# Kernel optimization log

Hardware: AMD Instinct MI355X
Metric: run time of the kernel (lower is better)

Reference implementation:

```python
import jax, jax.numpy as jnp
import numpy as np

BETA = 0.001       # gamma of the soft-min
THRESHOLD = 2.0    # padding cost for 'skip' slots


def _build_cost(centers_a, centers_b):
    # sort by timestamp (last column), then drop it (keep_times=False)
    a = centers_a[jnp.argsort(centers_a[:, -1])][:, :-1]
    b = centers_b[jnp.argsort(centers_b[:, -1])][:, :-1]
    a = a / jnp.sqrt(jnp.sum(a * a, axis=-1, keepdims=True) + 1e-10)
    b = b / jnp.sqrt(jnp.sum(b * b, axis=-1, keepdims=True) + 1e-10)
    cost = 1.0 - a @ b.T                      # [M, N] cosine cost
    M, N = cost.shape
    # interleave real costs with threshold 'skip' columns: [M, 2N]
    c2 = jnp.concatenate([cost, jnp.full_like(cost, THRESHOLD)], axis=0)  # [2M, N]
    c3 = c2.T.reshape(2 * N, M).T                                         # [M, 2N]
    c4 = jnp.concatenate(
        [jnp.full((M, 1), THRESHOLD, dtype=cost.dtype), c3], axis=1)      # [M, 2N+1]
    return jax.nn.softmax(c4, axis=-1)  # softmax='row'


def _dwsa_loss(C, gamma):
    # C: [M, K] with K = 2N+1. DP: D[i,j] = softmin(D[i-1, :p_j]) + C[i,j]
    # where p_j = j+1 for even j, j for odd j (prefix soft-min of previous row).
    M, K = C.shape
    j = jnp.arange(K)
    idx = jnp.where(j % 2 == 0, j, j - 1)  # inclusive prefix end index

    def step(d_prev, c_row):
        # stable prefix soft-min via cumulative logsumexp of -D/gamma
        lcse = jax.lax.cumlogsumexp(-d_prev / gamma)   # [K]
        softmin = -gamma * lcse[idx]                   # [K]
        d = softmin + c_row
        return d, None

    d_last, _ = jax.lax.scan(step, C[0], C[1:])
    # final soft-min over last row
    return -gamma * jax.nn.logsumexp(-d_last / gamma)


def setup_inputs() -> dict:
    key = jax.random.key(0)
    k1, k2 = jax.random.split(key)
    centers_a = jax.random.normal(k1, (2048, 513), dtype=jnp.float32)
    centers_b = jax.random.normal(k2, (2048, 513), dtype=jnp.float32)
    return {"centers_a": centers_a, "centers_b": centers_b}


def reference(centers_a, centers_b):
    C = _build_cost(centers_a, centers_b)
    return _dwsa_loss(C, BETA)
```

## Files before the change

### kernel.cpp

```cpp
#include <hip/hip_runtime.h>
#include <math.h>

#define M_ROWS 2048
#define N_COLS 2048
#define DIMS 512
#define IN_STRIDE 513
#define DP_BLOCKS 32
#define DP_COLS 64
#define BAND 16

constexpr float GAMMA = 0.001f;
constexpr float LOG2E = 1.44269504088896f;
constexpr float LN2   = 0.69314718055995f;

__device__ __forceinline__ float fexp2(float x) { return __builtin_amdgcn_exp2f(x); }
__device__ __forceinline__ float flog2(float x) { return __builtin_amdgcn_logf(x); }

__device__ __forceinline__ unsigned short f2bf(float x) {
    unsigned u = __float_as_uint(x);
    return (unsigned short)((u + 0x7FFFu + ((u >> 16) & 1u)) >> 16);
}
__device__ __forceinline__ float bf2f(unsigned short u) {
    return __uint_as_float((unsigned)u << 16);
}

__global__ void argsort_kernel(const float* __restrict__ a, const float* __restrict__ b,
                               int* __restrict__ permA, int* __restrict__ permB) {
    const float* src = blockIdx.y ? b : a;
    int* perm = blockIdx.y ? permB : permA;
    __shared__ float keys[M_ROWS];
    for (int j = threadIdx.x; j < M_ROWS; j += blockDim.x)
        keys[j] = src[(size_t)j * IN_STRIDE + DIMS];
    __syncthreads();
    int i = blockIdx.x * blockDim.x + threadIdx.x;
    float ki = keys[i];
    int rank = 0;
    for (int j = 0; j < M_ROWS; ++j) {
        float kj = keys[j];
        rank += (kj < ki) || (kj == ki && j < i);
    }
    perm[rank] = i;
}

__global__ __launch_bounds__(128) void norm_kernel(const float* __restrict__ a, const float* __restrict__ b,
                                                   const int* __restrict__ permA, const int* __restrict__ permB,
                                                   unsigned short* __restrict__ Ahi, unsigned short* __restrict__ Alo,
                                                   unsigned short* __restrict__ Bhi, unsigned short* __restrict__ Blo) {
    const float* src = blockIdx.y ? b : a;
    const int* perm = blockIdx.y ? permB : permA;
    unsigned short* dhi = blockIdx.y ? Bhi : Ahi;
    unsigned short* dlo = blockIdx.y ? Blo : Alo;
    int r = blockIdx.x;
    int row = perm[r];
    const float* p = src + (size_t)row * IN_STRIDE;
    int tid = threadIdx.x;
    float v0 = p[tid], v1 = p[tid + 128], v2 = p[tid + 256], v3 = p[tid + 384];
    float ss = v0 * v0 + v1 * v1 + v2 * v2 + v3 * v3;
    #pragma unroll
    for (int off = 32; off > 0; off >>= 1) ss += __shfl_down(ss, off);
    __shared__ float red[2];
    if ((tid & 63) == 0) red[tid >> 6] = ss;
    __syncthreads();
    float inv = 1.0f / sqrtf(red[0] + red[1] + 1e-10f);
    unsigned short* qh = dhi + (size_t)r * DIMS;
    unsigned short* ql = dlo + (size_t)r * DIMS;
    float x;
    unsigned short h;
    x = v0 * inv; h = f2bf(x); qh[tid]       = h; ql[tid]       = f2bf(x - bf2f(h));
    x = v1 * inv; h = f2bf(x); qh[tid + 128] = h; ql[tid + 128] = f2bf(x - bf2f(h));
    x = v2 * inv; h = f2bf(x); qh[tid + 256] = h; ql[tid + 256] = f2bf(x - bf2f(h));
    x = v3 * inv; h = f2bf(x); qh[tid + 384] = h; ql[tid + 384] = f2bf(x - bf2f(h));
}

typedef __attribute__((ext_vector_type(8))) short bf16x8;
typedef __attribute__((ext_vector_type(4))) float f32x4;

__global__ __launch_bounds__(256) void gemm_kernel(const unsigned short* __restrict__ Ahi,
                                                   const unsigned short* __restrict__ Alo,
                                                   const unsigned short* __restrict__ Bhi,
                                                   const unsigned short* __restrict__ Blo,
                                                   float* __restrict__ Q) {
    const int tid = threadIdx.x;
    const int lane = tid & 63;
    const int wv = tid >> 6;
    const int row0 = blockIdx.y * 64 + (wv >> 1) * 32;
    const int col0 = blockIdx.x * 64 + (wv & 1) * 32;
    const int lr = lane & 15;
    const int kj = (lane >> 4) * 8;
    const size_t ar0 = (size_t)(row0 + lr) * DIMS + kj;
    const size_t ar1 = (size_t)(row0 + 16 + lr) * DIMS + kj;
    const size_t br0 = (size_t)(col0 + lr) * DIMS + kj;
    const size_t br1 = (size_t)(col0 + 16 + lr) * DIMS + kj;
    f32x4 acc00 = {}, acc01 = {}, acc10 = {}, acc11 = {};
    for (int k0 = 0; k0 < DIMS; k0 += 32) {
        bf16x8 a0h = *(const bf16x8*)(Ahi + ar0 + k0);
        bf16x8 a1h = *(const bf16x8*)(Ahi + ar1 + k0);
        bf16x8 a0l = *(const bf16x8*)(Alo + ar0 + k0);
        bf16x8 a1l = *(const bf16x8*)(Alo + ar1 + k0);
        bf16x8 b0h = *(const bf16x8*)(Bhi + br0 + k0);
        bf16x8 b1h = *(const bf16x8*)(Bhi + br1 + k0);
        bf16x8 b0l = *(const bf16x8*)(Blo + br0 + k0);
        bf16x8 b1l = *(const bf16x8*)(Blo + br1 + k0);
        acc00 = __builtin_amdgcn_mfma_f32_16x16x32_bf16(a0l, b0h, acc00, 0, 0, 0);
        acc00 = __builtin_amdgcn_mfma_f32_16x16x32_bf16(a0h, b0l, acc00, 0, 0, 0);
        acc00 = __builtin_amdgcn_mfma_f32_16x16x32_bf16(a0h, b0h, acc00, 0, 0, 0);
        acc01 = __builtin_amdgcn_mfma_f32_16x16x32_bf16(a0l, b1h, acc01, 0, 0, 0);
        acc01 = __builtin_amdgcn_mfma_f32_16x16x32_bf16(a0h, b1l, acc01, 0, 0, 0);
        acc01 = __builtin_amdgcn_mfma_f32_16x16x32_bf16(a0h, b1h, acc01, 0, 0, 0);
        acc10 = __builtin_amdgcn_mfma_f32_16x16x32_bf16(a1l, b0h, acc10, 0, 0, 0);
        acc10 = __builtin_amdgcn_mfma_f32_16x16x32_bf16(a1h, b0l, acc10, 0, 0, 0);
        acc10 = __builtin_amdgcn_mfma_f32_16x16x32_bf16(a1h, b0h, acc10, 0, 0, 0);
        acc11 = __builtin_amdgcn_mfma_f32_16x16x32_bf16(a1l, b1h, acc11, 0, 0, 0);
        acc11 = __builtin_amdgcn_mfma_f32_16x16x32_bf16(a1h, b1l, acc11, 0, 0, 0);
        acc11 = __builtin_amdgcn_mfma_f32_16x16x32_bf16(a1h, b1h, acc11, 0, 0, 0);
    }
    const int rbase = (lane >> 4) * 4;
    #pragma unroll
    for (int r = 0; r < 4; ++r) {
        Q[(size_t)(row0 + rbase + r) * N_COLS + col0 + lr]           = __expf(-1.0f - acc00[r]);
        Q[(size_t)(row0 + rbase + r) * N_COLS + col0 + 16 + lr]      = __expf(-1.0f - acc01[r]);
        Q[(size_t)(row0 + 16 + rbase + r) * N_COLS + col0 + lr]      = __expf(-1.0f - acc10[r]);
        Q[(size_t)(row0 + 16 + rbase + r) * N_COLS + col0 + 16 + lr] = __expf(-1.0f - acc11[r]);
    }
}

__global__ __launch_bounds__(256) void rowstat_kernel(const float* __restrict__ Q,
                                                      float* __restrict__ rowscale,
                                                      float* __restrict__ ews) {
    int i = blockIdx.x;
    const float* q = Q + (size_t)i * N_COLS;
    int tid = threadIdx.x;
    float4 x = *(const float4*)(q + tid * 4);
    float4 y = *(const float4*)(q + 1024 + tid * 4);
    float s = x.x + x.y + x.z + x.w + y.x + y.y + y.z + y.w;
    #pragma unroll
    for (int off = 32; off > 0; off >>= 1) s += __shfl_down(s, off);
    __shared__ float red[4];
    if ((tid & 63) == 0) red[tid >> 6] = s;
    __syncthreads();
    if (tid == 0) {
        float denom = 2049.0f + red[0] + red[1] + red[2] + red[3];
        float rs = (LOG2E / GAMMA) / denom;
        rowscale[i] = rs;
        ews[i] = fexp2(-rs);
    }
}

__global__ __launch_bounds__(256) void lgt_kernel(const float* __restrict__ Q,
                                                  const float* __restrict__ rowscale,
                                                  float* __restrict__ ELT) {
    __shared__ float tile[64][65];
    const int row0 = blockIdx.y * 64;
    const int col0 = blockIdx.x * 64;
    const int t = threadIdx.x;
    const int c4 = (t & 15) * 4;
    const int r  = t >> 4;
    #pragma unroll
    for (int rr = 0; rr < 64; rr += 16) {
        int row = row0 + rr + r;
        float rs = rowscale[row];
        float4 v = *(const float4*)(Q + (size_t)row * N_COLS + col0 + c4);
        float e = fexp2(-rs);
        tile[c4 + 0][rr + r] = e + fexp2(-rs * v.x);
        tile[c4 + 1][rr + r] = e + fexp2(-rs * v.y);
        tile[c4 + 2][rr + r] = e + fexp2(-rs * v.z);
        tile[c4 + 3][rr + r] = e + fexp2(-rs * v.w);
    }
    __syncthreads();
    #pragma unroll
    for (int cc = 0; cc < 64; cc += 16) {
        int col = cc + r;
        float4 o;
        o.x = tile[col][c4 + 0];
        o.y = tile[col][c4 + 1];
        o.z = tile[col][c4 + 2];
        o.w = tile[col][c4 + 3];
        *(float4*)(ELT + (size_t)(col0 + col) * M_ROWS + row0 + c4) = o;
    }
}

#define KEEP4(v) asm volatile("" : "+v"(v.x), "+v"(v.y), "+v"(v.z), "+v"(v.w))

#define SST(V, MODS) asm("s_nop 1\n\tv_add_f32_dpp %0, %0, %0 " MODS : "+v"(V))
#define SCAN6                                                            \
    SST(t, "row_shr:1 row_mask:0xf bank_mask:0xf bound_ctrl:0");         \
    SST(t, "row_shr:2 row_mask:0xf bank_mask:0xf bound_ctrl:0");         \
    SST(t, "row_shr:4 row_mask:0xf bank_mask:0xf bound_ctrl:0");         \
    SST(t, "row_shr:8 row_mask:0xf bank_mask:0xf bound_ctrl:0");         \
    SST(t, "row_bcast:15 row_mask:0xa bank_mask:0xf bound_ctrl:0");      \
    SST(t, "row_bcast:31 row_mask:0xc bank_mask:0xf bound_ctrl:0")

#define DP_ROW(U, ELV, EWV, VCI)                                                 \
    {                                                                            \
        float ci = 0.f;                                                          \
        if (s > 0)                                                               \
            ci = __int_as_float(__builtin_amdgcn_readlane(                       \
                     __float_as_int(VCI), (U)));                                 \
        float t = w * (ELV);                                                     \
        float pre = fmaf(w, (EWV) - (ELV), ci);                                  \
        SCAN6;                                                                   \
        float all = ci + t;                                                      \
        float wn = pre + t;                                                      \
        if (s < DP_BLOCKS - 1) {                                                 \
            if (lane == 63) {                                                    \
                unsigned long long po =                                          \
                    ((unsigned long long)__float_as_uint(all) << 32)             \
                    | (unsigned long long)__float_as_uint(Rm);                   \
                __hip_atomic_store(pub + base + (U), po, __ATOMIC_RELAXED,       \
                                   __HIP_MEMORY_SCOPE_AGENT);                    \
            }                                                                    \
        } else {                                                                 \
            h = fmaf(h, (EWV), all);                                             \
        }                                                                        \
        w = wn;                                                                  \
    }

#define RENORM8                                                                  \
    {                                                                            \
        int e48 = __builtin_amdgcn_readlane(__builtin_amdgcn_frexp_expf(w), 48); \
        float f = __int_as_float((127 - e48) << 23);                             \
        w *= f; h *= f;                                                          \
        Rm += (float)e48;                                                        \
    }

#define WAIT_BAND                                                                \
    if (s > 0) {                                                                 \
        for (;;) {                                                               \
            unsigned long long miss = __ballot((lane < BAND) && pk == 0ull);     \
            if (miss == 0ull) break;                                             \
            if (pk == 0ull && lane < BAND)                                       \
                pk = __hip_atomic_load(sub + base + lane, __ATOMIC_RELAXED,      \
                                       __HIP_MEMORY_SCOPE_AGENT);               \
        }                                                                        \
        pkLo = (int)(unsigned)(pk & 0xFFFFFFFFull);                              \
        pkHi = (int)(unsigned)(pk >> 32);                                        \
    }

__global__ __launch_bounds__(64) void dp_kernel(const float* __restrict__ ELT,
                                                const float* __restrict__ Ews,
                                                unsigned long long* __restrict__ carry,
                                                float* __restrict__ out) {
    const int s = ((blockIdx.x & 7) << 2) | (blockIdx.x >> 3);
    const int lane = threadIdx.x;
    const float* lcol = ELT + (size_t)(s * DP_COLS + lane) * M_ROWS;
    unsigned long long* pub = carry + (size_t)s * M_ROWS;
    const unsigned long long* sub = carry + (size_t)(s - 1) * M_ROWS;

    float w = 1.f;
    float Rm = 0.f;
    float h = 1.f;

    float4 lq0 = *(const float4*)(lcol + 0);
    float4 lq1 = *(const float4*)(lcol + 4);
    float4 lq2 = *(const float4*)(lcol + 8);
    float4 lq3 = *(const float4*)(lcol + 12);
    float4 ev0 = *(const float4*)(Ews + 0);
    float4 ev1 = *(const float4*)(Ews + 4);
    float4 ev2 = *(const float4*)(Ews + 8);
    float4 ev3 = *(const float4*)(Ews + 12);
    KEEP4(lq0); KEEP4(lq1); KEEP4(lq2); KEEP4(lq3);
    KEEP4(ev0); KEEP4(ev1); KEEP4(ev2); KEEP4(ev3);

    unsigned long long pk = 1ull;
    if (s > 0 && lane < BAND)
        pk = __hip_atomic_load(sub + lane, __ATOMIC_RELAXED, __HIP_MEMORY_SCOPE_AGENT);

    for (int base = 0; base < M_ROWS; base += BAND) {
        float4 nl0{}, nl1{}, nl2{}, nl3{}, nv0{}, nv1{}, nv2{}, nv3{};
        if (base + BAND < M_ROWS) {
            nl0 = *(const float4*)(lcol + base + BAND);
            nl1 = *(const float4*)(lcol + base + BAND + 4);
            nl2 = *(const float4*)(lcol + base + BAND + 8);
            nl3 = *(const float4*)(lcol + base + BAND + 12);
            nv0 = *(const float4*)(Ews + base + BAND);
            nv1 = *(const float4*)(Ews + base + BAND + 4);
            nv2 = *(const float4*)(Ews + base + BAND + 8);
            nv3 = *(const float4*)(Ews + base + BAND + 12);
        }
        KEEP4(nl0); KEEP4(nl1); KEEP4(nl2); KEEP4(nl3);
        KEEP4(nv0); KEEP4(nv1); KEEP4(nv2); KEEP4(nv3);

        int pkLo = 0, pkHi = 0;
        WAIT_BAND
        float vci01 = 0.f;
        if (s > 0)
            vci01 = __int_as_float(pkHi) * fexp2(
                __int_as_float(__builtin_amdgcn_readlane(pkLo, 0)) - Rm);

        DP_ROW(0,  lq0.x, ev0.x, vci01)
        DP_ROW(1,  lq0.y, ev0.y, vci01)
        DP_ROW(2,  lq0.z, ev0.z, vci01)
        DP_ROW(3,  lq0.w, ev0.w, vci01)
        DP_ROW(4,  lq1.x, ev1.x, vci01)
        DP_ROW(5,  lq1.y, ev1.y, vci01)
        DP_ROW(6,  lq1.z, ev1.z, vci01)
        DP_ROW(7,  lq1.w, ev1.w, vci01)
        RENORM8
        float vci23 = 0.f;
        if (s > 0)
            vci23 = __int_as_float(pkHi) * fexp2(
                __int_as_float(__builtin_amdgcn_readlane(pkLo, 8)) - Rm);
        unsigned long long nk = 1ull;
        if (s > 0 && lane < BAND && base + BAND < M_ROWS)
            nk = __hip_atomic_load(sub + base + BAND + lane,
                                   __ATOMIC_RELAXED, __HIP_MEMORY_SCOPE_AGENT);

        DP_ROW(8,  lq2.x, ev2.x, vci23)
        DP_ROW(9,  lq2.y, ev2.y, vci23)
        DP_ROW(10, lq2.z, ev2.z, vci23)
        DP_ROW(11, lq2.w, ev2.w, vci23)
        DP_ROW(12, lq3.x, ev3.x, vci23)
        DP_ROW(13, lq3.y, ev3.y, vci23)
        DP_ROW(14, lq3.z, ev3.z, vci23)
        DP_ROW(15, lq3.w, ev3.w, vci23)
        RENORM8
        pk = nk;

        lq0 = nl0; lq1 = nl1; lq2 = nl2; lq3 = nl3;
        ev0 = nv0; ev1 = nv1; ev2 = nv2; ev3 = nv3;
    }
    if (s == DP_BLOCKS - 1 && lane == 63)
        out[0] = -GAMMA * LN2 * (Rm + flog2(h));
}

extern "C" void kernel_launch(void* const* d_in, const int* in_sizes, int n_in,
                              void* d_out, int out_size, void* d_ws, size_t ws_size,
                              hipStream_t stream) {
    (void)in_sizes; (void)n_in; (void)out_size; (void)ws_size;
    const float* a = (const float*)d_in[0];
    const float* b = (const float*)d_in[1];
    float* out = (float*)d_out;
    char* ws = (char*)d_ws;
    float* Q        = (float*)(ws);
    float* ELT      = (float*)(ws + (size_t)16 * 1024 * 1024);
    unsigned short* Ahi = (unsigned short*)(ws + (size_t)32 * 1024 * 1024);
    unsigned short* Alo = (unsigned short*)(ws + (size_t)34 * 1024 * 1024);
    unsigned short* Bhi = (unsigned short*)(ws + (size_t)36 * 1024 * 1024);
    unsigned short* Blo = (unsigned short*)(ws + (size_t)38 * 1024 * 1024);
    float* rowscale = (float*)(ws + (size_t)40 * 1024 * 1024);
    int* permA      = (int*)(ws + (size_t)40 * 1024 * 1024 + 8192);
    int* permB      = (int*)(ws + (size_t)40 * 1024 * 1024 + 16384);
    float* ews      = (float*)(ws + (size_t)40 * 1024 * 1024 + 24576);
    unsigned long long* carry = (unsigned long long*)(ws + (size_t)41 * 1024 * 1024);

    hipMemsetAsync(carry, 0, (size_t)DP_BLOCKS * M_ROWS * sizeof(unsigned long long), stream);
    argsort_kernel<<<dim3(8, 2), 256, 0, stream>>>(a, b, permA, permB);
    norm_kernel<<<dim3(2048, 2), 128, 0, stream>>>(a, b, permA, permB, Ahi, Alo, Bhi, Blo);
    gemm_kernel<<<dim3(32, 32), 256, 0, stream>>>(Ahi, Alo, Bhi, Blo, Q);
    rowstat_kernel<<<2048, 256, 0, stream>>>(Q, rowscale, ews);
    lgt_kernel<<<dim3(32, 32), 256, 0, stream>>>(Q, rowscale, ELT);
    dp_kernel<<<DP_BLOCKS, DP_COLS, 0, stream>>>(ELT, ews, carry, out);
}
```

Before: 582.4 us.

## Split DP band wait into halves, vectorize norm I/O, defer prefetch fences

The wavefront DP now waits only for the first eight carry values from the previous column block before starting, and polls for the second half during the first eight rows. This lets each block begin earlier in the pipeline. The norm kernel reads four contiguous floats per thread and writes ushort4 vectors, and the readlane of the carry is no longer guarded on s>0. The KEEP4 register fences are moved after the band so the prefetch loads can complete later. The changed carry handshake risks subtle ordering issues, and the unguarded readlane relies on vci being zero for block 0.

```diff
diff --git a/kernel.cpp b/kernel.cpp
--- a/kernel.cpp
+++ b/kernel.cpp
@@ -54,7 +54,7 @@
     int row = perm[r];
     const float* p = src + (size_t)row * IN_STRIDE;
     int tid = threadIdx.x;
-    float v0 = p[tid], v1 = p[tid + 128], v2 = p[tid + 256], v3 = p[tid + 384];
+    float v0 = p[4 * tid], v1 = p[4 * tid + 1], v2 = p[4 * tid + 2], v3 = p[4 * tid + 3];
     float ss = v0 * v0 + v1 * v1 + v2 * v2 + v3 * v3;
     #pragma unroll
     for (int off = 32; off > 0; off >>= 1) ss += __shfl_down(ss, off);
@@ -62,14 +62,14 @@
     if ((tid & 63) == 0) red[tid >> 6] = ss;
     __syncthreads();
     float inv = 1.0f / sqrtf(red[0] + red[1] + 1e-10f);
-    unsigned short* qh = dhi + (size_t)r * DIMS;
-    unsigned short* ql = dlo + (size_t)r * DIMS;
-    float x;
-    unsigned short h;
-    x = v0 * inv; h = f2bf(x); qh[tid]       = h; ql[tid]       = f2bf(x - bf2f(h));
-    x = v1 * inv; h = f2bf(x); qh[tid + 128] = h; ql[tid + 128] = f2bf(x - bf2f(h));
-    x = v2 * inv; h = f2bf(x); qh[tid + 256] = h; ql[tid + 256] = f2bf(x - bf2f(h));
-    x = v3 * inv; h = f2bf(x); qh[tid + 384] = h; ql[tid + 384] = f2bf(x - bf2f(h));
+    float x0 = v0 * inv, x1 = v1 * inv, x2 = v2 * inv, x3 = v3 * inv;
+    ushort4 hv, lv;
+    hv.x = f2bf(x0); lv.x = f2bf(x0 - bf2f(hv.x));
+    hv.y = f2bf(x1); lv.y = f2bf(x1 - bf2f(hv.y));
+    hv.z = f2bf(x2); lv.z = f2bf(x2 - bf2f(hv.z));
+    hv.w = f2bf(x3); lv.w = f2bf(x3 - bf2f(hv.w));
+    *(ushort4*)(dhi + (size_t)r * DIMS + 4 * tid) = hv;
+    *(ushort4*)(dlo + (size_t)r * DIMS + 4 * tid) = lv;
 }
 
 typedef __attribute__((ext_vector_type(8))) short bf16x8;
@@ -192,10 +192,8 @@
 
 #define DP_ROW(U, ELV, EWV, VCI)                                                 \
     {                                                                            \
-        float ci = 0.f;                                                          \
-        if (s > 0)                                                               \
-            ci = __int_as_float(__builtin_amdgcn_readlane(                       \
-                     __float_as_int(VCI), (U)));                                 \
+        float ci = __int_as_float(__builtin_amdgcn_readlane(                     \
+                       __float_as_int(VCI), (U)));                               \
         float t = w * (ELV);                                                     \
         float pre = fmaf(w, (EWV) - (ELV), ci);                                  \
         SCAN6;                                                                   \
@@ -223,12 +221,13 @@
         Rm += (float)e48;                                                        \
     }
 
-#define WAIT_BAND                                                                \
+#define WAIT_HALF(hh)                                                            \
     if (s > 0) {                                                                 \
         for (;;) {                                                               \
-            unsigned long long miss = __ballot((lane < BAND) && pk == 0ull);     \
+            unsigned long long miss =                                            \
+                __ballot(((lane >> 3) == (hh)) && pk == 0ull);                   \
             if (miss == 0ull) break;                                             \
-            if (pk == 0ull && lane < BAND)                                       \
+            if (pk == 0ull && lane < BAND && (lane >> 3) >= (hh))                \
                 pk = __hip_atomic_load(sub + base + lane, __ATOMIC_RELAXED,      \
                                        __HIP_MEMORY_SCOPE_AGENT);               \
         }                                                                        \
@@ -277,11 +276,9 @@
             nv2 = *(const float4*)(Ews + base + BAND + 8);
             nv3 = *(const float4*)(Ews + base + BAND + 12);
         }
-        KEEP4(nl0); KEEP4(nl1); KEEP4(nl2); KEEP4(nl3);
-        KEEP4(nv0); KEEP4(nv1); KEEP4(nv2); KEEP4(nv3);
 
         int pkLo = 0, pkHi = 0;
-        WAIT_BAND
+        WAIT_HALF(0)
         float vci01 = 0.f;
         if (s > 0)
             vci01 = __int_as_float(pkHi) * fexp2(
@@ -290,24 +287,28 @@
         DP_ROW(0,  lq0.x, ev0.x, vci01)
         DP_ROW(1,  lq0.y, ev0.y, vci01)
         DP_ROW(2,  lq0.z, ev0.z, vci01)
+        if (s > 0 && pk == 0ull && (lane >> 3) == 1)
+            pk = __hip_atomic_load(sub + base + lane, __ATOMIC_RELAXED,
+                                   __HIP_MEMORY_SCOPE_AGENT);
         DP_ROW(3,  lq0.w, ev0.w, vci01)
         DP_ROW(4,  lq1.x, ev1.x, vci01)
         DP_ROW(5,  lq1.y, ev1.y, vci01)
         DP_ROW(6,  lq1.z, ev1.z, vci01)
         DP_ROW(7,  lq1.w, ev1.w, vci01)
         RENORM8
+        WAIT_HALF(1)
         float vci23 = 0.f;
         if (s > 0)
             vci23 = __int_as_float(pkHi) * fexp2(
                 __int_as_float(__builtin_amdgcn_readlane(pkLo, 8)) - Rm);
+
+        DP_ROW(8,  lq2.x, ev2.x, vci23)
+        DP_ROW(9,  lq2.y, ev2.y, vci23)
+        DP_ROW(10, lq2.z, ev2.z, vci23)
         unsigned long long nk = 1ull;
         if (s > 0 && lane < BAND && base + BAND < M_ROWS)
             nk = __hip_atomic_load(sub + base + BAND + lane,
                                    __ATOMIC_RELAXED, __HIP_MEMORY_SCOPE_AGENT);
-
-        DP_ROW(8,  lq2.x, ev2.x, vci23)
-        DP_ROW(9,  lq2.y, ev2.y, vci23)
-        DP_ROW(10, lq2.z, ev2.z, vci23)
         DP_ROW(11, lq2.w, ev2.w, vci23)
         DP_ROW(12, lq3.x, ev3.x, vci23)
         DP_ROW(13, lq3.y, ev3.y, vci23)
@@ -316,6 +317,8 @@
         RENORM8
         pk = nk;
 
+        KEEP4(nl0); KEEP4(nl1); KEEP4(nl2); KEEP4(nl3);
+        KEEP4(nv0); KEEP4(nv1); KEEP4(nv2); KEEP4(nv3);
         lq0 = nl0; lq1 = nl1; lq2 = nl2; lq3 = nl3;
         ev0 = nv0; ev1 = nv1; ev2 = nv2; ev3 = nv3;
     }
```

After: 647.4 us. 11.2% more time.
